# Kernel tuning notes

Hardware: AMD Instinct MI355X
Metric: run time of the kernel (lower is better)

Reference implementation:

```python
import jax, jax.numpy as jnp
import numpy as np
from jax import lax

K = 3          # kernel_size
OUT = 256      # out_channels
IN_CPG = 256   # in_channels // groups
GROUPS = 1
STRIDE = 1
PAD = 1
DN = ('NCHW', 'OIHW', 'NCHW')


def _bounds(i, n, o):
    return int(np.floor(i * n / o)), int(np.ceil((i + 1) * n / o))


def adaptive_pool2d(x, o, reduce_fn):
    # Faithful torch AdaptiveAvg/MaxPool2d: static bin boundaries.
    H, W = x.shape[2], x.shape[3]
    rows = []
    for i in range(o):
        r0, r1 = _bounds(i, H, o)
        cells = []
        for j in range(o):
            c0, c1 = _bounds(j, W, o)
            cells.append(reduce_fn(x[:, :, r0:r1, c0:c1], axis=(2, 3)))
        rows.append(jnp.stack(cells, axis=-1))
    return jnp.stack(rows, axis=-2)  # (B, C, o, o)


def _gconv(x, w, fg, pad='VALID'):
    return lax.conv_general_dilated(x, w, (1, 1), pad,
                                    dimension_numbers=DN,
                                    feature_group_count=fg)


def setup_inputs() -> dict:
    key = jax.random.key(0)
    ks = jax.random.split(key, 7)
    s = 0.05
    return {
        'x':     jax.random.normal(ks[0], (32, 256, 56, 56), jnp.float32),
        'w1':    jax.random.normal(ks[1], (IN_CPG, GROUPS, 3, 3), jnp.float32) * s,
        'b1':    jax.random.normal(ks[2], (IN_CPG,), jnp.float32) * s,
        'w2':    jax.random.normal(ks[3], (OUT * IN_CPG, 1, 1, 1), jnp.float32) * s,
        'b2':    jax.random.normal(ks[4], (OUT * IN_CPG,), jnp.float32) * s,
        'w_att': jax.random.normal(ks[5], (OUT * IN_CPG, GROUPS, 3, 3), jnp.float32) * s,
        'b_att': jax.random.normal(ks[6], (OUT * IN_CPG,), jnp.float32) * s,
    }


def reference(x, w1, b1, w2, b2, w_att, b_att):
    B, C, H, W = x.shape
    # attention branch: maxpool -> grouped 3x3 conv -> sigmoid
    maxi = adaptive_pool2d(x, K + 2, jnp.max)                    # (B, C, K+2, K+2)
    att = _gconv(maxi, w_att, IN_CPG) + b_att[None, :, None, None]  # (B, OUT*IN_CPG, K, K)
    att = jax.nn.sigmoid(att).reshape(B * OUT, IN_CPG, K, K)
    # weight branch: avgpool -> depthwise 3x3 -> relu -> grouped 1x1
    avg = adaptive_pool2d(x, K + 2, jnp.mean)                    # (B, C, K+2, K+2)
    wgt = jax.nn.relu(_gconv(avg, w1, IN_CPG) + b1[None, :, None, None])  # (B, IN_CPG, K, K)
    wgt = _gconv(wgt, w2, IN_CPG) + b2[None, :, None, None]      # (B, OUT*IN_CPG, K, K)
    wgt = wgt.reshape(B * OUT, IN_CPG, K, K)
    # per-sample dynamic conv as grouped conv with batch-as-groups
    xg = x.reshape(1, B * C, H, W)
    out = lax.conv_general_dilated(xg, wgt * att, (STRIDE, STRIDE),
                                   [(PAD, PAD), (PAD, PAD)],
                                   dimension_numbers=DN,
                                   feature_group_count=GROUPS * B)
    return out.reshape(B, OUT, out.shape[-2], out.shape[-1])
```

## Files before the change

kernel.cpp:

```cpp
#include <hip/hip_runtime.h>
#include <hip/hip_bf16.h>

#define BATCH 32
#define CIN   256
#define OCH   256
#define HW    56
#define PW    58
#define PAREA (PW*PW)
#define PLANE (HW*HW)

typedef float float4v __attribute__((ext_vector_type(4)));
typedef short short8  __attribute__((ext_vector_type(8)));

__device__ __forceinline__ unsigned short f2bf(float f) {
  union { float f; unsigned u; } v; v.f = f;
  unsigned r = v.u + 0x7fffu + ((v.u >> 16) & 1u);
  return (unsigned short)(r >> 16);
}

__device__ __forceinline__ void gll16(const unsigned short* g, unsigned short* l) {
  __builtin_amdgcn_global_load_lds(
      (const __attribute__((address_space(1))) void*)g,
      (__attribute__((address_space(3))) void*)l,
      16, 0, 0);
}

__global__ __launch_bounds__(1024) void poolprep_kernel(
    const float* __restrict__ x, float* __restrict__ avgp,
    float* __restrict__ maxp, unsigned short* __restrict__ xp) {
  __shared__ float pl[8][3140];
  int bid = blockIdx.x;
  int cg = bid & 31, b = bid >> 5;
  int tid = threadIdx.x;
  const float* src = x + ((size_t)(b * 256 + cg * 8)) * PLANE;

  float4v v[7];
#pragma unroll
  for (int k = 0; k < 7; ++k) {
    int e = tid + k * 1024;
    if (e < 6272) v[k] = *(const float4v*)&src[(size_t)(e / 784) * PLANE + (e % 784) * 4];
  }
#pragma unroll
  for (int k = 0; k < 7; ++k) {
    int e = tid + k * 1024;
    if (e < 6272) *(float4v*)&pl[e / 784][(e % 784) * 4] = v[k];
  }
  __syncthreads();

  if (tid < 200) {
    int c = tid / 25, bin = tid % 25;
    int i = bin / 5, j = bin % 5;
    int r0 = (i * HW) / 5, r1 = ((i + 1) * HW + 4) / 5;
    int c0 = (j * HW) / 5, c1 = ((j + 1) * HW + 4) / 5;
    float s = 0.f, m = -1e30f;
    for (int r = r0; r < r1; ++r)
      for (int c2 = c0; c2 < c1; ++c2) {
        float vv = pl[c][r * HW + c2];
        s += vv; m = fmaxf(m, vv);
      }
    size_t o = ((size_t)(b * 256 + cg * 8 + c)) * 25 + bin;
    avgp[o] = s / (float)((r1 - r0) * (c1 - c0));
    maxp[o] = m;
  }

  int g32 = cg >> 2, cc = cg & 3;
  for (int p = tid; p < PLANE; p += 1024) {
    int y = p / 56, col = p % 56;
    int pos = (y + 1) * PW + (col + 1);
    short8 w8;
#pragma unroll
    for (int k = 0; k < 8; ++k) w8[k] = (short)f2bf(pl[k][p]);
    int cph = cc ^ ((pos >> 1) & 3);
    *(short8*)&xp[((size_t)b * PAREA + pos) * 256 + g32 * 32 + cph * 8] = w8;
  }
}

__global__ __launch_bounds__(256) void wcalc_kernel(
    const float* __restrict__ avgp, const float* __restrict__ maxp,
    const float* __restrict__ w1, const float* __restrict__ b1,
    const float* __restrict__ w2, const float* __restrict__ b2,
    const float* __restrict__ watt, const float* __restrict__ batt,
    unsigned short* __restrict__ Wbf) {
  int blk = blockIdx.x;
  int oc = blk & 255, b = blk >> 8;
  __shared__ float s_avg[25], s_max[25], s_w1[9], s_wgt1[9];
  int tid = threadIdx.x;
  size_t base = ((size_t)b * 256 + oc) * 25;
  if (tid < 25) { s_avg[tid] = avgp[base + tid]; s_max[tid] = maxp[base + tid]; }
  if (tid >= 32 && tid < 41) s_w1[tid - 32] = w1[oc * 9 + (tid - 32)];
  __syncthreads();
  if (tid < 9) {
    int ky = tid / 3, kx = tid % 3;
    float acc = b1[oc];
    for (int u = 0; u < 3; ++u)
      for (int v = 0; v < 3; ++v)
        acc += s_avg[(ky + u) * 5 + kx + v] * s_w1[u * 3 + v];
    s_wgt1[tid] = fmaxf(acc, 0.f);
  }
  __syncthreads();
  int ic = tid;
  size_t g = (size_t)oc * 256 + ic;
  float wa[9];
#pragma unroll
  for (int r = 0; r < 9; ++r) wa[r] = watt[g * 9 + r];
  float ba = batt[g], w2v = w2[g], b2v = b2[g];

  int ocb = oc >> 7, ocl = oc & 127;
  int icb = ic >> 5;
  size_t tilebase = ((size_t)((b * 2 + ocb) * 8 + icb)) * 9;
  size_t elem = (size_t)ocl * 32 + (ic & 31);

#pragma unroll
  for (int r = 0; r < 9; ++r) {
    int ky = r / 3, kx = r % 3;
    float s = ba;
#pragma unroll
    for (int u = 0; u < 3; ++u)
#pragma unroll
      for (int v = 0; v < 3; ++v)
        s += s_max[(ky + u) * 5 + kx + v] * wa[u * 3 + v];
    float att = 1.f / (1.f + __expf(-s));
    float wv = (s_wgt1[r] * w2v + b2v) * att;
    Wbf[(tilebase + r) * 4096 + elem] = f2bf(wv);
  }
}

__global__ __launch_bounds__(256) void border_kernel(unsigned short* __restrict__ xp) {
  int bid = blockIdx.x;
  int b = bid / 228, bi = bid % 228;
  int pos;
  if (bi < 58)       pos = bi;
  else if (bi < 116) pos = 57 * PW + (bi - 58);
  else if (bi < 172) pos = (bi - 116 + 1) * PW;
  else               pos = (bi - 172 + 1) * PW + 57;
  xp[((size_t)b * PAREA + pos) * 256 + threadIdx.x] = 0;
}

__global__ __launch_bounds__(256, 2) void conv_kernel(
    const unsigned short* __restrict__ xp,
    const unsigned short* __restrict__ Wbf,
    float* __restrict__ out) {
  __shared__ unsigned short bpl[2][348 * 32];

  int p = blockIdx.x;
  int L = (p & 7) * 112 + (p >> 3);
  int rt = L % 14; int t2 = L / 14; int ocb = t2 & 1; int b = t2 >> 1;
  int y0 = rt * 4;
  int tid = threadIdx.x;
  int lane = tid & 63, w = tid >> 6;
  int mw = w & 1, nw = w >> 1;
  int quad = lane >> 4, l16 = lane & 15;

  int basepos[7];
#pragma unroll
  for (int nt = 0; nt < 7; ++nt) {
    int n = nw * 112 + nt * 16 + l16;
    basepos[nt] = (n / 56) * PW + (n % 56);
  }

  float4v acc[4][7];
#pragma unroll
  for (int mt = 0; mt < 4; ++mt)
#pragma unroll
    for (int nt = 0; nt < 7; ++nt)
      acc[mt][nt] = (float4v){0.f, 0.f, 0.f, 0.f};

  const size_t xbase = ((size_t)b * PAREA + (size_t)y0 * PW) * 256;
  const unsigned short* wb = Wbf + (size_t)((b * 2 + ocb) * 72) * 4096;
  const int aoff = (mw * 64 + l16) * 32 + quad * 8;

  for (int e = tid; e < 1392; e += 256)
    gll16(&xp[xbase + (size_t)(e >> 2) * 256 + (e & 3) * 8], &bpl[0][e * 8]);
  __syncthreads();

  for (int icb = 0; icb < 8; ++icb) {
    int cur = icb & 1;
    if (icb < 7) {
      for (int e = tid; e < 1392; e += 256)
        gll16(&xp[xbase + (size_t)(e >> 2) * 256 + (icb + 1) * 32 + (e & 3) * 8],
              &bpl[cur ^ 1][e * 8]);
    }
    const unsigned short* wt = wb + (size_t)icb * 9 * 4096;
#pragma unroll
    for (int r = 0; r < 9; ++r) {
      short8 af[4];
#pragma unroll
      for (int mt = 0; mt < 4; ++mt)
        af[mt] = *(const short8*)&wt[(size_t)r * 4096 + mt * 512 + aoff];
      int ky = r / 3, kx = r - ky * 3;
      int po = ky * PW + kx;
      short8 bfrag[7];
#pragma unroll
      for (int nt = 0; nt < 7; ++nt) {
        int pr = basepos[nt] + po;
        bfrag[nt] = *(const short8*)&bpl[cur][pr * 32 + ((quad ^ ((pr >> 1) & 3)) << 3)];
      }
#pragma unroll
      for (int mt = 0; mt < 4; ++mt)
#pragma unroll
        for (int nt = 0; nt < 7; ++nt)
          acc[mt][nt] = __builtin_amdgcn_mfma_f32_16x16x32_bf16(af[mt], bfrag[nt], acc[mt][nt], 0, 0, 0);
    }
    __syncthreads();
  }

#pragma unroll
  for (int mt = 0; mt < 4; ++mt) {
    int m = ocb * 128 + mw * 64 + mt * 16 + quad * 4;
#pragma unroll
    for (int nt = 0; nt < 7; ++nt) {
      int n = nw * 112 + nt * 16 + l16;
      int yy = y0 + n / 56, xx = n % 56;
      size_t o = (((size_t)b * 256 + m) * 56 + yy) * 56 + xx;
#pragma unroll
      for (int reg = 0; reg < 4; ++reg)
        out[o + (size_t)reg * PLANE] = acc[mt][nt][reg];
    }
  }
}

extern "C" void kernel_launch(void* const* d_in, const int* in_sizes, int n_in,
                              void* d_out, int out_size, void* d_ws, size_t ws_size,
                              hipStream_t stream) {
  const float* x    = (const float*)d_in[0];
  const float* w1   = (const float*)d_in[1];
  const float* b1   = (const float*)d_in[2];
  const float* w2   = (const float*)d_in[3];
  const float* b2   = (const float*)d_in[4];
  const float* watt = (const float*)d_in[5];
  const float* batt = (const float*)d_in[6];
  float* out = (float*)d_out;

  float* avgp = (float*)d_ws;
  float* maxp = avgp + 204800;
  unsigned short* Wbf = (unsigned short*)(maxp + 204800);
  unsigned short* xp  = Wbf + (size_t)32 * 9 * 256 * 256;

  poolprep_kernel<<<BATCH * 32, 1024, 0, stream>>>(x, avgp, maxp, xp);
  wcalc_kernel<<<BATCH * OCH, 256, 0, stream>>>(avgp, maxp, w1, b1, w2, b2, watt, batt, Wbf);
  border_kernel<<<BATCH * 228, 256, 0, stream>>>(xp);
  conv_kernel<<<BATCH * 2 * 14, 256, 0, stream>>>(xp, Wbf, out);
}
```

Before: 475.2 us.

## Prefetch conv weight fragments two taps ahead and split poolprep into smaller blocks

After: 740.9 us. 55.9% more time.

```diff
diff --git a/kernel.cpp b/kernel.cpp
--- a/kernel.cpp
+++ b/kernel.cpp
@@ -11,6 +11,7 @@
 
 typedef float float4v __attribute__((ext_vector_type(4)));
 typedef short short8  __attribute__((ext_vector_type(8)));
+typedef short short4v __attribute__((ext_vector_type(4)));
 
 __device__ __forceinline__ unsigned short f2bf(float f) {
   union { float f; unsigned u; } v; v.f = f;
@@ -25,29 +26,30 @@
       16, 0, 0);
 }
 
-__global__ __launch_bounds__(1024) void poolprep_kernel(
+__global__ __launch_bounds__(512) void poolprep_kernel(
     const float* __restrict__ x, float* __restrict__ avgp,
     float* __restrict__ maxp, unsigned short* __restrict__ xp) {
-  __shared__ float pl[8][3140];
-  int bid = blockIdx.x;
-  int cg = bid & 31, b = bid >> 5;
+  __shared__ float pl[4][3140];
+  int p = blockIdx.x;
+  int L = (p & 7) * 256 + (p >> 3);
+  int cg = L & 63, b = L >> 6;
   int tid = threadIdx.x;
-  const float* src = x + ((size_t)(b * 256 + cg * 8)) * PLANE;
+  const float* src = x + ((size_t)(b * 256 + cg * 4)) * PLANE;
 
   float4v v[7];
 #pragma unroll
   for (int k = 0; k < 7; ++k) {
-    int e = tid + k * 1024;
-    if (e < 6272) v[k] = *(const float4v*)&src[(size_t)(e / 784) * PLANE + (e % 784) * 4];
+    int e = tid + k * 512;
+    if (e < 3136) v[k] = *(const float4v*)&src[(size_t)(e / 784) * PLANE + (e % 784) * 4];
   }
 #pragma unroll
   for (int k = 0; k < 7; ++k) {
-    int e = tid + k * 1024;
-    if (e < 6272) *(float4v*)&pl[e / 784][(e % 784) * 4] = v[k];
-  }
-  __syncthreads();
-
-  if (tid < 200) {
+    int e = tid + k * 512;
+    if (e < 3136) *(float4v*)&pl[e / 784][(e % 784) * 4] = v[k];
+  }
+  __syncthreads();
+
+  if (tid < 100) {
     int c = tid / 25, bin = tid % 25;
     int i = bin / 5, j = bin % 5;
     int r0 = (i * HW) / 5, r1 = ((i + 1) * HW + 4) / 5;
@@ -58,20 +60,23 @@
         float vv = pl[c][r * HW + c2];
         s += vv; m = fmaxf(m, vv);
       }
-    size_t o = ((size_t)(b * 256 + cg * 8 + c)) * 25 + bin;
+    size_t o = ((size_t)(b * 256 + cg * 4 + c)) * 25 + bin;
     avgp[o] = s / (float)((r1 - r0) * (c1 - c0));
     maxp[o] = m;
   }
 
-  int g32 = cg >> 2, cc = cg & 3;
-  for (int p = tid; p < PLANE; p += 1024) {
-    int y = p / 56, col = p % 56;
+  int ch0 = cg * 4;
+  int g32 = ch0 >> 5;
+  int cc = (ch0 >> 3) & 3;
+  int half = (ch0 >> 2) & 1;
+  for (int pi = tid; pi < PLANE; pi += 512) {
+    int y = pi / 56, col = pi % 56;
     int pos = (y + 1) * PW + (col + 1);
-    short8 w8;
-#pragma unroll
-    for (int k = 0; k < 8; ++k) w8[k] = (short)f2bf(pl[k][p]);
+    short4v w4;
+#pragma unroll
+    for (int k = 0; k < 4; ++k) w4[k] = (short)f2bf(pl[k][pi]);
     int cph = cc ^ ((pos >> 1) & 3);
-    *(short8*)&xp[((size_t)b * PAREA + pos) * 256 + g32 * 32 + cph * 8] = w8;
+    *(short4v*)&xp[((size_t)b * PAREA + pos) * 256 + g32 * 32 + cph * 8 + half * 4] = w4;
   }
 }
 
@@ -171,8 +176,46 @@
 
   for (int e = tid; e < 1392; e += 256)
     gll16(&xp[xbase + (size_t)(e >> 2) * 256 + (e & 3) * 8], &bpl[0][e * 8]);
-  __syncthreads();
-
+  short8 afA0, afA1, afA2, afA3, afB0, afB1, afB2, afB3;
+  {
+    const unsigned short* w0p = wb + aoff;
+    afA0 = *(const short8*)&w0p[0];    afA1 = *(const short8*)&w0p[512];
+    afA2 = *(const short8*)&w0p[1024]; afA3 = *(const short8*)&w0p[1536];
+    const unsigned short* w1p = wb + 4096 + aoff;
+    afB0 = *(const short8*)&w1p[0];    afB1 = *(const short8*)&w1p[512];
+    afB2 = *(const short8*)&w1p[1024]; afB3 = *(const short8*)&w1p[1536];
+  }
+  __syncthreads();
+
+#define RSTEP(R, S, ICB, CUR) do {                                              \
+    const int _po = ((R) / 3) * PW + ((R) % 3);                                 \
+    short8 _bf[7];                                                              \
+    _Pragma("unroll")                                                           \
+    for (int nt = 0; nt < 7; ++nt) {                                            \
+      int pr = basepos[nt] + _po;                                               \
+      _bf[nt] = *(const short8*)&bpl[CUR][pr * 32 + ((quad ^ ((pr >> 1) & 3)) << 3)]; \
+    }                                                                           \
+    const int _kk2 = (ICB) * 9 + (R) + 2;                                       \
+    const unsigned short* _w2 = wb + (size_t)_kk2 * 4096 + aoff;                \
+    _Pragma("unroll")                                                           \
+    for (int nt = 0; nt < 7; ++nt)                                              \
+      acc[0][nt] = __builtin_amdgcn_mfma_f32_16x16x32_bf16(S##0, _bf[nt], acc[0][nt], 0, 0, 0); \
+    if (_kk2 < 72) S##0 = *(const short8*)&_w2[0];                              \
+    _Pragma("unroll")                                                           \
+    for (int nt = 0; nt < 7; ++nt)                                              \
+      acc[1][nt] = __builtin_amdgcn_mfma_f32_16x16x32_bf16(S##1, _bf[nt], acc[1][nt], 0, 0, 0); \
+    if (_kk2 < 72) S##1 = *(const short8*)&_w2[512];                            \
+    _Pragma("unroll")                                                           \
+    for (int nt = 0; nt < 7; ++nt)                                              \
+      acc[2][nt] = __builtin_amdgcn_mfma_f32_16x16x32_bf16(S##2, _bf[nt], acc[2][nt], 0, 0, 0); \
+    if (_kk2 < 72) S##2 = *(const short8*)&_w2[1024];                           \
+    _Pragma("unroll")                                                           \
+    for (int nt = 0; nt < 7; ++nt)                                              \
+      acc[3][nt] = __builtin_amdgcn_mfma_f32_16x16x32_bf16(S##3, _bf[nt], acc[3][nt], 0, 0, 0); \
+    if (_kk2 < 72) S##3 = *(const short8*)&_w2[1536];                           \
+  } while (0)
+
+#pragma unroll 1
   for (int icb = 0; icb < 8; ++icb) {
     int cur = icb & 1;
     if (icb < 7) {
@@ -180,29 +223,18 @@
         gll16(&xp[xbase + (size_t)(e >> 2) * 256 + (icb + 1) * 32 + (e & 3) * 8],
               &bpl[cur ^ 1][e * 8]);
     }
-    const unsigned short* wt = wb + (size_t)icb * 9 * 4096;
-#pragma unroll
-    for (int r = 0; r < 9; ++r) {
-      short8 af[4];
-#pragma unroll
-      for (int mt = 0; mt < 4; ++mt)
-        af[mt] = *(const short8*)&wt[(size_t)r * 4096 + mt * 512 + aoff];
-      int ky = r / 3, kx = r - ky * 3;
-      int po = ky * PW + kx;
-      short8 bfrag[7];
-#pragma unroll
-      for (int nt = 0; nt < 7; ++nt) {
-        int pr = basepos[nt] + po;
-        bfrag[nt] = *(const short8*)&bpl[cur][pr * 32 + ((quad ^ ((pr >> 1) & 3)) << 3)];
-      }
-#pragma unroll
-      for (int mt = 0; mt < 4; ++mt)
-#pragma unroll
-        for (int nt = 0; nt < 7; ++nt)
-          acc[mt][nt] = __builtin_amdgcn_mfma_f32_16x16x32_bf16(af[mt], bfrag[nt], acc[mt][nt], 0, 0, 0);
+    if (!(icb & 1)) {
+      RSTEP(0, afA, icb, cur); RSTEP(1, afB, icb, cur); RSTEP(2, afA, icb, cur);
+      RSTEP(3, afB, icb, cur); RSTEP(4, afA, icb, cur); RSTEP(5, afB, icb, cur);
+      RSTEP(6, afA, icb, cur); RSTEP(7, afB, icb, cur); RSTEP(8, afA, icb, cur);
+    } else {
+      RSTEP(0, afB, icb, cur); RSTEP(1, afA, icb, cur); RSTEP(2, afB, icb, cur);
+      RSTEP(3, afA, icb, cur); RSTEP(4, afB, icb, cur); RSTEP(5, afA, icb, cur);
+      RSTEP(6, afB, icb, cur); RSTEP(7, afA, icb, cur); RSTEP(8, afB, icb, cur);
     }
     __syncthreads();
   }
+#undef RSTEP
 
 #pragma unroll
   for (int mt = 0; mt < 4; ++mt) {
@@ -236,7 +268,7 @@
   unsigned short* Wbf = (unsigned short*)(maxp + 204800);
   unsigned short* xp  = Wbf + (size_t)32 * 9 * 256 * 256;
 
-  poolprep_kernel<<<BATCH * 32, 1024, 0, stream>>>(x, avgp, maxp, xp);
+  poolprep_kernel<<<BATCH * 64, 512, 0, stream>>>(x, avgp, maxp, xp);
   wcalc_kernel<<<BATCH * OCH, 256, 0, stream>>>(avgp, maxp, w1, b1, w2, b2, watt, batt, Wbf);
   border_kernel<<<BATCH * 228, 256, 0, stream>>>(xp);
   conv_kernel<<<BATCH * 2 * 14, 256, 0, stream>>>(xp, Wbf, out);
```
